# Performance work log

Measured on AMD Instinct MI355X. Metric: run time of the kernel, lower is better.

Reference implementation:

```python
import jax, jax.numpy as jnp
import numpy as np

B, T = 32, 64
DETER, HID, STOCH, CLASSES = 2048, 1024, 32, 32
ACT, EMB, BLOCKS = 16, 1024, 8
FLAT = STOCH * CLASSES
DPB = DETER // BLOCKS
DYN_IN_PB = DPB + 3 * HID
EPS = 1e-6
UNIMIX = 0.01


def _rms(x, g):
    return x * jax.lax.rsqrt(jnp.mean(x * x, axis=-1, keepdims=True) + EPS) * g


def _block_linear(x, W, b):
    # x: [N, BLOCKS*in_pb], W: [BLOCKS, in_pb, out_pb] -> [N, BLOCKS*out_pb]
    xg = x.reshape(x.shape[0], BLOCKS, -1)
    y = jnp.einsum('nbi,bio->nbo', xg, W)
    return y.reshape(x.shape[0], -1) + b


def setup_inputs() -> dict:
    key = jax.random.key(0)
    ks = iter(jax.random.split(key, 64))
    def lin(i, o):
        return jax.random.normal(next(ks), (i, o), jnp.float32) / np.float32(np.sqrt(i))
    inp = {}
    inp['embed'] = jax.random.normal(next(ks), (B, T, EMB), jnp.float32)
    inp['action'] = jax.random.normal(next(ks), (B, T, ACT), jnp.float32)
    inp['is_first'] = jax.random.randint(next(ks), (B, T), 0, 2).astype(jnp.int32)
    inp['W_in_deter'] = lin(DETER, HID); inp['b_in_deter'] = jnp.zeros((HID,), jnp.float32); inp['g_in_deter'] = jnp.ones((HID,), jnp.float32)
    inp['W_in_stoch'] = lin(FLAT, HID); inp['b_in_stoch'] = jnp.zeros((HID,), jnp.float32); inp['g_in_stoch'] = jnp.ones((HID,), jnp.float32)
    inp['W_in_act'] = lin(ACT, HID); inp['b_in_act'] = jnp.zeros((HID,), jnp.float32); inp['g_in_act'] = jnp.ones((HID,), jnp.float32)
    inp['W_dyn'] = jax.random.normal(next(ks), (BLOCKS, DYN_IN_PB, DPB), jnp.float32) / np.float32(np.sqrt(DYN_IN_PB))
    inp['b_dyn'] = jnp.zeros((DETER,), jnp.float32); inp['g_dyn'] = jnp.ones((DETER,), jnp.float32)
    inp['W_gru'] = jax.random.normal(next(ks), (BLOCKS, DPB, 3 * DPB), jnp.float32) / np.float32(np.sqrt(DPB))
    inp['b_gru'] = jnp.zeros((3 * DETER,), jnp.float32)
    inp['W_p0'] = lin(DETER, HID); inp['b_p0'] = jnp.zeros((HID,), jnp.float32); inp['g_p0'] = jnp.ones((HID,), jnp.float32)
    inp['W_p1'] = lin(HID, HID); inp['b_p1'] = jnp.zeros((HID,), jnp.float32); inp['g_p1'] = jnp.ones((HID,), jnp.float32)
    inp['W_po'] = jax.random.uniform(next(ks), (HID, FLAT), jnp.float32, -1.0, 1.0) / np.float32(np.sqrt(HID))
    inp['b_po'] = jnp.zeros((FLAT,), jnp.float32)
    inp['W_q0'] = lin(DETER + EMB, HID); inp['b_q0'] = jnp.zeros((HID,), jnp.float32); inp['g_q0'] = jnp.ones((HID,), jnp.float32)
    inp['W_qo'] = jax.random.uniform(next(ks), (HID, FLAT), jnp.float32, -1.0, 1.0) / np.float32(np.sqrt(HID))
    inp['b_qo'] = jnp.zeros((FLAT,), jnp.float32)
    return inp


def reference(embed, action, is_first,
              W_in_deter, b_in_deter, g_in_deter,
              W_in_stoch, b_in_stoch, g_in_stoch,
              W_in_act, b_in_act, g_in_act,
              W_dyn, b_dyn, g_dyn, W_gru, b_gru,
              W_p0, b_p0, g_p0, W_p1, b_p1, g_p1, W_po, b_po,
              W_q0, b_q0, g_q0, W_qo, b_qo):

    def core(deter, stoch_flat, act):
        denom = jax.lax.stop_gradient(jnp.maximum(jnp.abs(act), 1.0))
        a = act / denom
        x0 = jax.nn.silu(_rms(deter @ W_in_deter + b_in_deter, g_in_deter))
        x1 = jax.nn.silu(_rms(stoch_flat @ W_in_stoch + b_in_stoch, g_in_stoch))
        x2 = jax.nn.silu(_rms(a @ W_in_act + b_in_act, g_in_act))
        x = jnp.concatenate([x0, x1, x2], axis=-1)  # [B, 3H]
        xb = jnp.broadcast_to(x[:, None, :], (x.shape[0], BLOCKS, 3 * HID))
        dg = deter.reshape(-1, BLOCKS, DPB)
        h = jnp.concatenate([dg, xb], axis=-1).reshape(x.shape[0], -1)
        h = jax.nn.silu(_rms(_block_linear(h, W_dyn, b_dyn), g_dyn))
        gates = _block_linear(h, W_gru, b_gru).reshape(-1, BLOCKS, 3 * DPB)
        r = jax.nn.sigmoid(gates[..., :DPB])
        c = jnp.tanh(r * gates[..., DPB:2 * DPB])
        u = jax.nn.sigmoid(gates[..., 2 * DPB:] - 1.0)
        return (u * c + (1.0 - u) * dg).reshape(-1, DETER)

    def prior(deter):
        x = jax.nn.silu(_rms(deter @ W_p0 + b_p0, g_p0))
        x = jax.nn.silu(_rms(x @ W_p1 + b_p1, g_p1))
        return (x @ W_po + b_po).reshape(-1, STOCH, CLASSES)

    def post(deter, emb):
        x = jnp.concatenate([deter, emb], axis=-1)
        x = jax.nn.silu(_rms(x @ W_q0 + b_q0, g_q0))
        return (x @ W_qo + b_qo).reshape(-1, STOCH, CLASSES)

    def mode_st(logits):
        # unimix categorical, deterministic mode with straight-through gradients
        probs = (1.0 - UNIMIX) * jax.nn.softmax(logits, axis=-1) + UNIMIX / CLASSES
        onehot = jax.nn.one_hot(jnp.argmax(probs, axis=-1), CLASSES, dtype=probs.dtype)
        return onehot + probs - jax.lax.stop_gradient(probs)

    def step(carry, xs):
        deter, stoch = carry
        emb_t, act_t, first_t = xs
        m = (1.0 - first_t.astype(jnp.float32))[:, None]
        deter = deter * m
        stoch = stoch * m
        act_t = act_t * m
        deter = core(deter, stoch, act_t)
        prior_logits = prior(deter)
        post_logits = post(deter, emb_t)
        stoch = mode_st(post_logits).reshape(-1, FLAT)
        return (deter, stoch), (post_logits, prior_logits, deter)

    carry0 = (jnp.zeros((B, DETER), embed.dtype), jnp.zeros((B, FLAT), embed.dtype))
    xs = (embed.transpose(1, 0, 2), action.transpose(1, 0, 2), is_first.T)
    _, (post_l, prior_l, deters) = jax.lax.scan(step, carry0, xs)
    return (post_l.transpose(1, 0, 2, 3), prior_l.transpose(1, 0, 2, 3), deters.transpose(1, 0, 2))
```

## Files before the change

kernel.cpp:

```cpp
#include <hip/hip_runtime.h>
#include <math.h>

#define DEVINL __device__ __forceinline__
typedef float f32x4 __attribute__((ext_vector_type(4)));


struct RPtrs {
  const float *embed, *action; const int *is_first;
  const float *W_in_deter, *b_in_deter, *g_in_deter;
  const float *W_in_stoch, *b_in_stoch, *g_in_stoch;
  const float *W_in_act,   *b_in_act,   *g_in_act;
  const float *W_dyn, *b_dyn, *g_dyn;
  const float *W_gru, *b_gru;
  const float *W_p0, *b_p0, *g_p0;
  const float *W_p1, *b_p1, *g_p1;
  const float *W_po, *b_po;
  const float *W_q0, *b_q0, *g_q0;
  const float *W_qo, *b_qo;
  float *out_post, *out_prior, *out_deters;
  float *deter, *determ, *xact, *hact, *q0act;
  float *SDyn, *SQ0, *SX0, *SQO, *Abuf0, *Abuf1;
};

struct LdPlain {
  const float* A; int lda;
  DEVINL const float* addr(int r, int k) const { return A + (size_t)r * lda + k; }
};
struct LdDyn {
  const float* dm; const float* x; int blk;
  DEVINL const float* addr(int r, int k) const {
    return (k < 256) ? dm + (size_t)r * 2048 + blk * 256 + k
                     : x + (size_t)r * 3072 + (k - 256);
  }
};
struct LdQ0 {
  const float* det; const float* emb; int t;
  DEVINL const float* addr(int r, int k) const {
    return (k < 2048) ? det + (size_t)r * 2048 + k
                      : emb + ((size_t)r * 64 + t) * 1024 + (k - 2048);
  }
};

#define FMA4(A, S, W) { (A)[0]=fmaf((S),(W)[0],(A)[0]); (A)[1]=fmaf((S),(W)[1],(A)[1]); \
                        (A)[2]=fmaf((S),(W)[2],(A)[2]); (A)[3]=fmaf((S),(W)[3],(A)[3]); }

template <int NBLK, typename LA>
DEVINL void gemm_tile(LA la, const float* __restrict__ W, int ldw, int wcb,
                      int k0, float* __restrict__ slab, int sst, int scb,
                      const float* __restrict__ bias, float* As) {
  const int tid = threadIdx.x;
  const int c4 = (tid & 63) * 4;
  const int rg = (tid >> 6) * 8;
  const int srr = tid & 31;
  const int skk = (tid >> 5) * 8;
  f32x4 acc[8];
#pragma unroll
  for (int i = 0; i < 8; ++i) acc[i] = (f32x4){0.f, 0.f, 0.f, 0.f};
  const float* ap = la.addr(srr, k0 + skk);
  f32x4 cur0 = *(const f32x4*)ap;
  f32x4 cur1 = *(const f32x4*)(ap + 4);
#pragma unroll
  for (int b = 0; b < NBLK; ++b) {
    __syncthreads();
#pragma unroll
    for (int e = 0; e < 4; ++e) {
      As[(skk + e) * 36 + srr]     = cur0[e];
      As[(skk + 4 + e) * 36 + srr] = cur1[e];
    }
    f32x4 nxt0, nxt1;
    if (b + 1 < NBLK) {
      const float* np = la.addr(srr, k0 + (b + 1) * 64 + skk);
      nxt0 = *(const f32x4*)np;
      nxt1 = *(const f32x4*)(np + 4);
    }
    __syncthreads();
    const float* Wp = W + (size_t)(k0 + b * 64) * ldw + wcb + c4;
#pragma unroll 8
    for (int kk = 0; kk < 64; ++kk) {
      f32x4 w = *(const f32x4*)(Wp + (size_t)kk * ldw);
      const float* Ab = As + kk * 36 + rg;
      f32x4 alo = *(const f32x4*)(Ab);
      f32x4 ahi = *(const f32x4*)(Ab + 4);
      FMA4(acc[0], alo[0], w); FMA4(acc[1], alo[1], w);
      FMA4(acc[2], alo[2], w); FMA4(acc[3], alo[3], w);
      FMA4(acc[4], ahi[0], w); FMA4(acc[5], ahi[1], w);
      FMA4(acc[6], ahi[2], w); FMA4(acc[7], ahi[3], w);
    }
    if (b + 1 < NBLK) { cur0 = nxt0; cur1 = nxt1; }
  }
  f32x4 bv = (f32x4){0.f, 0.f, 0.f, 0.f};
  if (bias) bv = *(const f32x4*)(bias + wcb + c4);
#pragma unroll
  for (int i = 0; i < 8; ++i) {
    f32x4 o = acc[i] + bv;
    *(f32x4*)(slab + (size_t)(rg + i) * sst + scb + c4) = o;
  }
}

template <typename LA>
DEVINL void gemm_big(LA la, const float* __restrict__ W, int ldw, int wcb,
                     int nblk, float* __restrict__ outp, int ost,
                     const float* __restrict__ bias, float* As) {
  const int tid = threadIdx.x;
  const int c4 = (tid & 63) * 4;
  const int rg = (tid >> 6) * 8;
  const int srr = tid & 31;
  const int skk = (tid >> 5) * 8;
  f32x4 acc[8];
#pragma unroll
  for (int i = 0; i < 8; ++i) acc[i] = (f32x4){0.f, 0.f, 0.f, 0.f};
  const float* ap = la.addr(srr, skk);
  f32x4 cur0 = *(const f32x4*)ap;
  f32x4 cur1 = *(const f32x4*)(ap + 4);
  f32x4 nxt0, nxt1;
  for (int b = 0; b < nblk; ++b) {
    __syncthreads();
#pragma unroll
    for (int e = 0; e < 4; ++e) {
      As[(skk + e) * 36 + srr]     = cur0[e];
      As[(skk + 4 + e) * 36 + srr] = cur1[e];
    }
    if (b + 1 < nblk) {
      const float* np = la.addr(srr, (b + 1) * 64 + skk);
      nxt0 = *(const f32x4*)np;
      nxt1 = *(const f32x4*)(np + 4);
    }
    __syncthreads();
    const float* Wp = W + (size_t)(b * 64) * ldw + wcb + c4;
#pragma unroll 8
    for (int kk = 0; kk < 64; ++kk) {
      f32x4 w = *(const f32x4*)(Wp + (size_t)kk * ldw);
      const float* Ab = As + kk * 36 + rg;
      f32x4 alo = *(const f32x4*)(Ab);
      f32x4 ahi = *(const f32x4*)(Ab + 4);
      FMA4(acc[0], alo[0], w); FMA4(acc[1], alo[1], w);
      FMA4(acc[2], alo[2], w); FMA4(acc[3], alo[3], w);
      FMA4(acc[4], ahi[0], w); FMA4(acc[5], ahi[1], w);
      FMA4(acc[6], ahi[2], w); FMA4(acc[7], ahi[3], w);
    }
    if (b + 1 < nblk) { cur0 = nxt0; cur1 = nxt1; }
  }
  f32x4 bv = *(const f32x4*)(bias + wcb + c4);
#pragma unroll
  for (int i = 0; i < 8; ++i) {
    f32x4 o = acc[i] + bv;
    *(f32x4*)(outp + (size_t)(rg + i) * ost + wcb + c4) = o;
  }
}

DEVINL void act_fin(const float* __restrict__ slab, int N, int nch, int r,
                    const float* __restrict__ g, float* __restrict__ out,
                    float invN, float* red) {
  const int tid = threadIdx.x;
  const size_t cstr = (size_t)32 * N;
  const float* base = slab + (size_t)r * N + tid * 4;
  f32x4 y0 = (f32x4){0.f, 0.f, 0.f, 0.f}, y1 = y0;
  for (int ch = 0; ch < nch; ++ch)
    y0 += *(const f32x4*)(base + (size_t)ch * cstr);
  float ss = y0[0]*y0[0] + y0[1]*y0[1] + y0[2]*y0[2] + y0[3]*y0[3];
  if (N == 2048) {
    for (int ch = 0; ch < nch; ++ch)
      y1 += *(const f32x4*)(base + 1024 + (size_t)ch * cstr);
    ss += y1[0]*y1[0] + y1[1]*y1[1] + y1[2]*y1[2] + y1[3]*y1[3];
  }
#pragma unroll
  for (int o = 32; o > 0; o >>= 1) ss += __shfl_down(ss, o, 64);
  if ((tid & 63) == 0) red[tid >> 6] = ss;
  __syncthreads();
  if (tid == 0)
    red[4] = 1.f / sqrtf((red[0] + red[1] + red[2] + red[3]) * invN + 1e-6f);
  __syncthreads();
  const float sc = red[4];
  {
    f32x4 gg = *(const f32x4*)(g + tid * 4);
    f32x4 v = y0 * sc * gg;
#pragma unroll
    for (int k = 0; k < 4; ++k) v[k] = v[k] / (1.f + expf(-v[k]));
    *(f32x4*)(out + tid * 4) = v;
  }
  if (N == 2048) {
    f32x4 gg = *(const f32x4*)(g + 1024 + tid * 4);
    f32x4 v = y1 * sc * gg;
#pragma unroll
    for (int k = 0; k < 4; ++k) v[k] = v[k] / (1.f + expf(-v[k]));
    *(f32x4*)(out + 1024 + tid * 4) = v;
  }
}

DEVINL float sigm(float x) { return 1.f / (1.f + expf(-x)); }

DEVINL void x2_row(const RPtrs& p, int tt, int r, float m, float* red) {
  const int tid = threadIdx.x;
  const int c0 = tid * 4;
  const float* arow = p.action + ((size_t)r * 64 + tt) * 16;
  f32x4 s2 = *(const f32x4*)(p.b_in_act + c0);
#pragma unroll
  for (int ii = 0; ii < 16; ++ii) {
    float av = arow[ii] * m;
    av = av / fmaxf(fabsf(av), 1.f);
    f32x4 wv = *(const f32x4*)(p.W_in_act + ii * 1024 + c0);
    FMA4(s2, av, wv);
  }
  float ss = s2[0]*s2[0] + s2[1]*s2[1] + s2[2]*s2[2] + s2[3]*s2[3];
#pragma unroll
  for (int o = 32; o > 0; o >>= 1) ss += __shfl_down(ss, o, 64);
  if ((tid & 63) == 0) red[tid >> 6] = ss;
  __syncthreads();
  if (tid == 0)
    red[4] = 1.f / sqrtf((red[0] + red[1] + red[2] + red[3]) * (1.f / 1024.f) + 1e-6f);
  __syncthreads();
  float sc = red[4];
  f32x4 gg = *(const f32x4*)(p.g_in_act + c0);
  f32x4 v = s2 * sc * gg;
#pragma unroll
  for (int k = 0; k < 4; ++k) v[k] = v[k] / (1.f + expf(-v[k]));
  *(f32x4*)(p.xact + (size_t)r * 3072 + 2048 + c0) = v;
}

__global__ __launch_bounds__(256) void k_init(RPtrs p) {
  size_t i = (size_t)blockIdx.x * 256 + threadIdx.x;
  if (i < 65536) { p.deter[i] = 0.f; p.determ[i] = 0.f; }
}

__global__ __launch_bounds__(256, 2) void k_x0p(RPtrs p) {
  __shared__ __align__(16) float As[2304];
  int ct = blockIdx.x & 3, kc = blockIdx.x >> 2;
  LdPlain la{p.determ, 2048};
  gemm_tile<2>(la, p.W_in_deter, 1024, ct * 256, kc * 128,
               p.SX0 + (size_t)kc * 32768, 1024, ct * 256,
               kc == 0 ? p.b_in_deter : nullptr, As);
}

__global__ __launch_bounds__(256, 2) void k_profin(RPtrs p) {
  __shared__ float red[8];
  const int wg = blockIdx.x;
  const int tid = threadIdx.x;
  if (wg < 32) {
    act_fin(p.SX0, 1024, 16, wg, p.g_in_deter, p.xact + (size_t)wg * 3072,
            1.f / 1024.f, red);
  } else {
    const int r = wg - 32;
    const int c0 = tid * 4;
    f32x4 pre = *(const f32x4*)(p.b_in_stoch + c0);
    float ss = pre[0]*pre[0] + pre[1]*pre[1] + pre[2]*pre[2] + pre[3]*pre[3];
#pragma unroll
    for (int o = 32; o > 0; o >>= 1) ss += __shfl_down(ss, o, 64);
    if ((tid & 63) == 0) red[tid >> 6] = ss;
    __syncthreads();
    if (tid == 0)
      red[4] = 1.f / sqrtf((red[0] + red[1] + red[2] + red[3]) * (1.f / 1024.f) + 1e-6f);
    __syncthreads();
    float sc = red[4];
    f32x4 gg = *(const f32x4*)(p.g_in_stoch + c0);
    f32x4 v = pre * sc * gg;
#pragma unroll
    for (int k = 0; k < 4; ++k) v[k] = v[k] / (1.f + expf(-v[k]));
    *(f32x4*)(p.xact + (size_t)r * 3072 + 1024 + c0) = v;
    __syncthreads();
    float m = p.is_first[r * 64] ? 0.f : 1.f;
    x2_row(p, 0, r, m, red);
  }
}

__global__ __launch_bounds__(256, 2) void k_dyn(RPtrs p, int t) {
  __shared__ __align__(16) float As[2304];
  const int wg = blockIdx.x;
  int blk = wg / 26, kc = wg % 26;
  LdDyn la{p.determ, p.xact, blk};
  gemm_tile<2>(la, p.W_dyn + (size_t)blk * 851968, 256, 0, kc * 128,
               p.SDyn + (size_t)kc * 65536, 2048, blk * 256,
               kc == 0 ? p.b_dyn + blk * 256 : nullptr, As);
}

__global__ __launch_bounds__(256, 2) void k_dynfin(RPtrs p) {
  __shared__ float red[8];
  act_fin(p.SDyn, 2048, 26, blockIdx.x, p.g_dyn,
          p.hact + (size_t)blockIdx.x * 2048, 1.f / 2048.f, red);
}

__global__ __launch_bounds__(256, 2) void k_gru(RPtrs p, int t) {
  __shared__ float Al[8704];
  const int wg = blockIdx.x;
  const int blk = wg >> 4, jch = wg & 15;
  const int tid = threadIdx.x;
  {
    const float* hp = p.hact + blk * 256 + tid;
#pragma unroll
    for (int jb = 0; jb < 32; ++jb)
      Al[tid * 34 + jb] = hp[(size_t)jb * 2048];
  }
  __syncthreads();
  const int j = tid & 15, rg = tid >> 4;
  const int r0 = rg * 2;
  const int jcol = jch * 16 + j;
  const float* Wg = p.W_gru + (size_t)blk * 196608 + jcol;
  float r0a = 0, r1a = 0, c0a = 0, c1a = 0, u0a = 0, u1a = 0;
#pragma unroll 4
  for (int kk = 0; kk < 256; ++kk) {
    float wr = Wg[(size_t)kk * 768];
    float wc = Wg[(size_t)kk * 768 + 256];
    float wu = Wg[(size_t)kk * 768 + 512];
    float ax = Al[kk * 34 + r0], ay = Al[kk * 34 + r0 + 1];
    r0a = fmaf(ax, wr, r0a); r1a = fmaf(ay, wr, r1a);
    c0a = fmaf(ax, wc, c0a); c1a = fmaf(ay, wc, c1a);
    u0a = fmaf(ax, wu, u0a); u1a = fmaf(ay, wu, u1a);
  }
  const int col = blk * 256 + jcol;
  const float br = p.b_gru[blk * 768 + jcol];
  const float bc = p.b_gru[blk * 768 + 256 + jcol];
  const float bu = p.b_gru[blk * 768 + 512 + jcol];
#pragma unroll
  for (int rr = 0; rr < 2; ++rr) {
    int r = r0 + rr;
    float gr = (rr ? r1a : r0a) + br;
    float gc = (rr ? c1a : c0a) + bc;
    float gu = (rr ? u1a : u0a) + bu;
    float rs = sigm(gr);
    float cc = tanhf(rs * gc);
    float uu = sigm(gu - 1.f);
    float dg = p.determ[(size_t)r * 2048 + col];
    float nd = uu * cc + (1.f - uu) * dg;
    p.deter[(size_t)r * 2048 + col] = nd;
    p.out_deters[((size_t)r * 64 + t) * 2048 + col] = nd;
    float mn = 0.f;
    if (t + 1 < 64) mn = p.is_first[r * 64 + (t + 1)] ? 0.f : 1.f;
    p.determ[(size_t)r * 2048 + col] = nd * mn;
  }
}

__global__ __launch_bounds__(256, 2) void k_q0x0(RPtrs p, int t) {
  __shared__ __align__(16) float As[2304];
  const int wg = blockIdx.x;
  if (wg < 96) {
    int ct = wg & 3, kc = wg >> 2;
    LdQ0 la{p.deter, p.embed, t};
    gemm_tile<2>(la, p.W_q0, 1024, ct * 256, kc * 128,
                 p.SQ0 + (size_t)kc * 32768, 1024, ct * 256,
                 kc == 0 ? p.b_q0 : nullptr, As);
  } else {
    if (t >= 63) return;
    int i = wg - 96, ct = i & 3, kc = i >> 2;
    LdPlain la{p.determ, 2048};
    gemm_tile<2>(la, p.W_in_deter, 1024, ct * 256, kc * 128,
                 p.SX0 + (size_t)kc * 32768, 1024, ct * 256,
                 kc == 0 ? p.b_in_deter : nullptr, As);
  }
}

__global__ __launch_bounds__(256, 2) void k_qfin(RPtrs p, int t) {
  __shared__ float red[8];
  const int wg = blockIdx.x;
  if (wg < 32)
    act_fin(p.SQ0, 1024, 24, wg, p.g_q0, p.q0act + (size_t)wg * 1024,
            1.f / 1024.f, red);
  else {
    if (t >= 63) return;
    act_fin(p.SX0, 1024, 16, wg - 32, p.g_in_deter,
            p.xact + (size_t)(wg - 32) * 3072, 1.f / 1024.f, red);
  }
}

__global__ __launch_bounds__(256, 2) void k_qo(RPtrs p, int t) {
  __shared__ __align__(16) float As[2304];
  int ct = blockIdx.x & 3, kc = blockIdx.x >> 2;
  LdPlain la{p.q0act, 1024};
  gemm_tile<1>(la, p.W_qo, 1024, ct * 256, kc * 64,
               p.SQO + (size_t)kc * 32768, 1024, ct * 256,
               kc == 0 ? p.b_qo : nullptr, As);
}

__global__ __launch_bounds__(256, 2) void k_finx12(RPtrs p, int t) {
  __shared__ __align__(16) float ybuf[1024];
  __shared__ float red[8];
  __shared__ int sidx[32];
  const int r = blockIdx.x;
  const int tid = threadIdx.x;
  const float* b0 = p.SQO + (size_t)r * 1024 + tid * 4;
  f32x4 y = (f32x4){0.f, 0.f, 0.f, 0.f};
#pragma unroll
  for (int ch = 0; ch < 16; ++ch) y += *(const f32x4*)(b0 + (size_t)ch * 32768);
  *(f32x4*)(p.out_post + ((size_t)r * 64 + t) * 1024 + tid * 4) = y;
  *(f32x4*)(ybuf + tid * 4) = y;
  __syncthreads();
  if (tid < 32) {
    const float* rb = ybuf + tid * 32;
    float best = rb[0]; int bi = 0;
#pragma unroll
    for (int c = 1; c < 32; ++c) {
      float v = rb[c];
      if (v > best) { best = v; bi = c; }
    }
    sidx[tid] = bi;
  }
  __syncthreads();
  if (t >= 63) return;
  const float m = p.is_first[r * 64 + t + 1] ? 0.f : 1.f;
  const int c0 = tid * 4;
  f32x4 s1 = (f32x4){0.f, 0.f, 0.f, 0.f};
  if (m != 0.f) {
    for (int g = 0; g < 32; ++g)
      s1 += *(const f32x4*)(p.W_in_stoch + (size_t)(g * 32 + sidx[g]) * 1024 + c0);
  }
  f32x4 pre = *(const f32x4*)(p.b_in_stoch + c0) + s1 * m;
  float ss = pre[0]*pre[0] + pre[1]*pre[1] + pre[2]*pre[2] + pre[3]*pre[3];
#pragma unroll
  for (int o = 32; o > 0; o >>= 1) ss += __shfl_down(ss, o, 64);
  if ((tid & 63) == 0) red[tid >> 6] = ss;
  __syncthreads();
  if (tid == 0)
    red[4] = 1.f / sqrtf((red[0] + red[1] + red[2] + red[3]) * (1.f / 1024.f) + 1e-6f);
  __syncthreads();
  {
    float sc = red[4];
    f32x4 gg = *(const f32x4*)(p.g_in_stoch + c0);
    f32x4 v = pre * sc * gg;
#pragma unroll
    for (int k = 0; k < 4; ++k) v[k] = v[k] / (1.f + expf(-v[k]));
    *(f32x4*)(p.xact + (size_t)r * 3072 + 1024 + c0) = v;
  }
  __syncthreads();
  x2_row(p, t + 1, r, m, red);
}

__global__ __launch_bounds__(256, 2) void kb_p0(RPtrs p) {
  __shared__ __align__(16) float As[2304];
  int rb = blockIdx.x >> 2, ct = blockIdx.x & 3;
  LdPlain la{p.out_deters + (size_t)rb * 32 * 2048, 2048};
  gemm_big(la, p.W_p0, 1024, ct * 256, 32,
           p.Abuf0 + (size_t)rb * 32 * 1024, 1024, p.b_p0, As);
}
__global__ __launch_bounds__(256, 2) void kb_fin0(RPtrs p) {
  __shared__ float red[8];
  int r = blockIdx.x;
  act_fin(p.Abuf0, 1024, 1, r, p.g_p0, p.Abuf1 + (size_t)r * 1024,
          1.f / 1024.f, red);
}
__global__ __launch_bounds__(256, 2) void kb_p1(RPtrs p) {
  __shared__ __align__(16) float As[2304];
  int rb = blockIdx.x >> 2, ct = blockIdx.x & 3;
  LdPlain la{p.Abuf1 + (size_t)rb * 32 * 1024, 1024};
  gemm_big(la, p.W_p1, 1024, ct * 256, 16,
           p.Abuf0 + (size_t)rb * 32 * 1024, 1024, p.b_p1, As);
}
__global__ __launch_bounds__(256, 2) void kb_fin1(RPtrs p) {
  __shared__ float red[8];
  int r = blockIdx.x;
  act_fin(p.Abuf0, 1024, 1, r, p.g_p1, p.Abuf1 + (size_t)r * 1024,
          1.f / 1024.f, red);
}
__global__ __launch_bounds__(256, 2) void kb_po(RPtrs p) {
  __shared__ __align__(16) float As[2304];
  int rb = blockIdx.x >> 2, ct = blockIdx.x & 3;
  LdPlain la{p.Abuf1 + (size_t)rb * 32 * 1024, 1024};
  gemm_big(la, p.W_po, 1024, ct * 256, 16,
           p.out_prior + (size_t)rb * 32 * 1024, 1024, p.b_po, As);
}

extern "C" void kernel_launch(void* const* d_in, const int* in_sizes, int n_in,
                              void* d_out, int out_size, void* d_ws,
                              size_t ws_size, hipStream_t stream) {
  RPtrs p;
  p.embed      = (const float*)d_in[0];
  p.action     = (const float*)d_in[1];
  p.is_first   = (const int*)d_in[2];
  p.W_in_deter = (const float*)d_in[3];  p.b_in_deter = (const float*)d_in[4];  p.g_in_deter = (const float*)d_in[5];
  p.W_in_stoch = (const float*)d_in[6];  p.b_in_stoch = (const float*)d_in[7];  p.g_in_stoch = (const float*)d_in[8];
  p.W_in_act   = (const float*)d_in[9];  p.b_in_act   = (const float*)d_in[10]; p.g_in_act   = (const float*)d_in[11];
  p.W_dyn      = (const float*)d_in[12]; p.b_dyn      = (const float*)d_in[13]; p.g_dyn      = (const float*)d_in[14];
  p.W_gru      = (const float*)d_in[15]; p.b_gru      = (const float*)d_in[16];
  p.W_p0       = (const float*)d_in[17]; p.b_p0       = (const float*)d_in[18]; p.g_p0       = (const float*)d_in[19];
  p.W_p1       = (const float*)d_in[20]; p.b_p1       = (const float*)d_in[21]; p.g_p1       = (const float*)d_in[22];
  p.W_po       = (const float*)d_in[23]; p.b_po       = (const float*)d_in[24];
  p.W_q0       = (const float*)d_in[25]; p.b_q0       = (const float*)d_in[26]; p.g_q0       = (const float*)d_in[27];
  p.W_qo       = (const float*)d_in[28]; p.b_qo       = (const float*)d_in[29];

  float* o = (float*)d_out;
  p.out_post   = o;
  p.out_prior  = o + 2097152;
  p.out_deters = o + 4194304;

  float* w = (float*)d_ws;
  p.deter  = w;
  p.determ = w + 65536;
  p.xact   = w + 131072;
  p.hact   = w + 229376;
  p.q0act  = w + 294912;
  p.SDyn   = w + 393216;
  p.SQ0    = w + 2097152;
  p.SX0    = w + 2883584;
  p.SQO    = w + 3407872;
  p.Abuf0  = w;
  p.Abuf1  = w + 2097152;

  k_init<<<512, 256, 0, stream>>>(p);
  k_x0p<<<64, 256, 0, stream>>>(p);
  k_profin<<<64, 256, 0, stream>>>(p);
  for (int t = 0; t < 64; ++t) {
    k_dyn<<<208, 256, 0, stream>>>(p, t);
    k_dynfin<<<32, 256, 0, stream>>>(p);
    k_gru<<<128, 256, 0, stream>>>(p, t);
    k_q0x0<<<160, 256, 0, stream>>>(p, t);
    k_qfin<<<64, 256, 0, stream>>>(p, t);
    k_qo<<<64, 256, 0, stream>>>(p, t);
    k_finx12<<<32, 256, 0, stream>>>(p, t);
  }
  kb_p0<<<256, 256, 0, stream>>>(p);
  kb_fin0<<<2048, 256, 0, stream>>>(p);
  kb_p1<<<256, 256, 0, stream>>>(p);
  kb_fin1<<<2048, 256, 0, stream>>>(p);
  kb_po<<<256, 256, 0, stream>>>(p);
}
```

Baseline: 7.257 ms.

## Fuse q-finalize, qo projection and stoch update into one per-row kernel

Merges the q0 RMS-norm finalize, the W_qo projection and the argmax/stoch embedding step into a single kernel per batch row. The qo projection becomes a per-row matrix-vector loop instead of a split-K GEMM with a partial-sum buffer. The initial x0 GEMM on zero state is replaced by computing the activation straight from the bias inside the init kernel. This cuts launches and intermediate buffers per timestep, but each of only 32 blocks now streams all of W_qo serially, which may lengthen the critical path.

```diff
diff --git a/kernel.cpp b/kernel.cpp
--- a/kernel.cpp
+++ b/kernel.cpp
@@ -18,8 +18,8 @@
   const float *W_q0, *b_q0, *g_q0;
   const float *W_qo, *b_qo;
   float *out_post, *out_prior, *out_deters;
-  float *deter, *determ, *xact, *hact, *q0act;
-  float *SDyn, *SQ0, *SX0, *SQO, *Abuf0, *Abuf1;
+  float *deter, *determ, *xact, *hact;
+  float *SDyn, *SQ0, *SX0, *Abuf0, *Abuf1;
 };
 
 struct LdPlain {
@@ -217,45 +217,37 @@
   *(f32x4*)(p.xact + (size_t)r * 3072 + 2048 + c0) = v;
 }
 
+DEVINL void bias_row(const float* __restrict__ b, const float* __restrict__ g,
+                     float* __restrict__ out, float* red) {
+  const int tid = threadIdx.x;
+  const int c0 = tid * 4;
+  f32x4 pre = *(const f32x4*)(b + c0);
+  float ss = pre[0]*pre[0] + pre[1]*pre[1] + pre[2]*pre[2] + pre[3]*pre[3];
+#pragma unroll
+  for (int o = 32; o > 0; o >>= 1) ss += __shfl_down(ss, o, 64);
+  if ((tid & 63) == 0) red[tid >> 6] = ss;
+  __syncthreads();
+  if (tid == 0)
+    red[4] = 1.f / sqrtf((red[0] + red[1] + red[2] + red[3]) * (1.f / 1024.f) + 1e-6f);
+  __syncthreads();
+  float sc = red[4];
+  f32x4 gg = *(const f32x4*)(g + c0);
+  f32x4 v = pre * sc * gg;
+#pragma unroll
+  for (int k = 0; k < 4; ++k) v[k] = v[k] / (1.f + expf(-v[k]));
+  *(f32x4*)(out + c0) = v;
+}
+
 __global__ __launch_bounds__(256) void k_init(RPtrs p) {
-  size_t i = (size_t)blockIdx.x * 256 + threadIdx.x;
-  if (i < 65536) { p.deter[i] = 0.f; p.determ[i] = 0.f; }
-}
-
-__global__ __launch_bounds__(256, 2) void k_x0p(RPtrs p) {
-  __shared__ __align__(16) float As[2304];
-  int ct = blockIdx.x & 3, kc = blockIdx.x >> 2;
-  LdPlain la{p.determ, 2048};
-  gemm_tile<2>(la, p.W_in_deter, 1024, ct * 256, kc * 128,
-               p.SX0 + (size_t)kc * 32768, 1024, ct * 256,
-               kc == 0 ? p.b_in_deter : nullptr, As);
-}
-
-__global__ __launch_bounds__(256, 2) void k_profin(RPtrs p) {
   __shared__ float red[8];
   const int wg = blockIdx.x;
-  const int tid = threadIdx.x;
-  if (wg < 32) {
-    act_fin(p.SX0, 1024, 16, wg, p.g_in_deter, p.xact + (size_t)wg * 3072,
-            1.f / 1024.f, red);
-  } else {
-    const int r = wg - 32;
-    const int c0 = tid * 4;
-    f32x4 pre = *(const f32x4*)(p.b_in_stoch + c0);
-    float ss = pre[0]*pre[0] + pre[1]*pre[1] + pre[2]*pre[2] + pre[3]*pre[3];
-#pragma unroll
-    for (int o = 32; o > 0; o >>= 1) ss += __shfl_down(ss, o, 64);
-    if ((tid & 63) == 0) red[tid >> 6] = ss;
-    __syncthreads();
-    if (tid == 0)
-      red[4] = 1.f / sqrtf((red[0] + red[1] + red[2] + red[3]) * (1.f / 1024.f) + 1e-6f);
-    __syncthreads();
-    float sc = red[4];
-    f32x4 gg = *(const f32x4*)(p.g_in_stoch + c0);
-    f32x4 v = pre * sc * gg;
-#pragma unroll
-    for (int k = 0; k < 4; ++k) v[k] = v[k] / (1.f + expf(-v[k]));
-    *(f32x4*)(p.xact + (size_t)r * 3072 + 1024 + c0) = v;
+  size_t i = (size_t)wg * 256 + threadIdx.x;
+  if (i < 65536) { p.deter[i] = 0.f; p.determ[i] = 0.f; }
+  if (wg >= 480) {
+    const int r = wg - 480;
+    bias_row(p.b_in_deter, p.g_in_deter, p.xact + (size_t)r * 3072, red);
+    __syncthreads();
+    bias_row(p.b_in_stoch, p.g_in_stoch, p.xact + (size_t)r * 3072 + 1024, red);
     __syncthreads();
     float m = p.is_first[r * 64] ? 0.f : 1.f;
     x2_row(p, 0, r, m, red);
@@ -347,41 +339,55 @@
   }
 }
 
-__global__ __launch_bounds__(256, 2) void k_qfin(RPtrs p, int t) {
+__global__ __launch_bounds__(256, 2) void k_mega(RPtrs p, int t) {
+  __shared__ __align__(16) float qrow[1024];
+  __shared__ __align__(16) float ybuf[1024];
   __shared__ float red[8];
+  __shared__ int sidx[32];
   const int wg = blockIdx.x;
-  if (wg < 32)
-    act_fin(p.SQ0, 1024, 24, wg, p.g_q0, p.q0act + (size_t)wg * 1024,
-            1.f / 1024.f, red);
-  else {
+  const int tid = threadIdx.x;
+  if (wg >= 32) {
     if (t >= 63) return;
     act_fin(p.SX0, 1024, 16, wg - 32, p.g_in_deter,
             p.xact + (size_t)(wg - 32) * 3072, 1.f / 1024.f, red);
-  }
-}
-
-__global__ __launch_bounds__(256, 2) void k_qo(RPtrs p, int t) {
-  __shared__ __align__(16) float As[2304];
-  int ct = blockIdx.x & 3, kc = blockIdx.x >> 2;
-  LdPlain la{p.q0act, 1024};
-  gemm_tile<1>(la, p.W_qo, 1024, ct * 256, kc * 64,
-               p.SQO + (size_t)kc * 32768, 1024, ct * 256,
-               kc == 0 ? p.b_qo : nullptr, As);
-}
-
-__global__ __launch_bounds__(256, 2) void k_finx12(RPtrs p, int t) {
-  __shared__ __align__(16) float ybuf[1024];
-  __shared__ float red[8];
-  __shared__ int sidx[32];
-  const int r = blockIdx.x;
-  const int tid = threadIdx.x;
-  const float* b0 = p.SQO + (size_t)r * 1024 + tid * 4;
-  f32x4 y = (f32x4){0.f, 0.f, 0.f, 0.f};
-#pragma unroll
-  for (int ch = 0; ch < 16; ++ch) y += *(const f32x4*)(b0 + (size_t)ch * 32768);
-  *(f32x4*)(p.out_post + ((size_t)r * 64 + t) * 1024 + tid * 4) = y;
-  *(f32x4*)(ybuf + tid * 4) = y;
-  __syncthreads();
+    return;
+  }
+  const int r = wg;
+  const int c0 = tid * 4;
+  {
+    const float* base = p.SQ0 + (size_t)r * 1024 + c0;
+    f32x4 y = (f32x4){0.f, 0.f, 0.f, 0.f};
+#pragma unroll
+    for (int ch = 0; ch < 24; ++ch) y += *(const f32x4*)(base + (size_t)ch * 32768);
+    float ss = y[0]*y[0] + y[1]*y[1] + y[2]*y[2] + y[3]*y[3];
+#pragma unroll
+    for (int o = 32; o > 0; o >>= 1) ss += __shfl_down(ss, o, 64);
+    if ((tid & 63) == 0) red[tid >> 6] = ss;
+    __syncthreads();
+    if (tid == 0)
+      red[4] = 1.f / sqrtf((red[0] + red[1] + red[2] + red[3]) * (1.f / 1024.f) + 1e-6f);
+    __syncthreads();
+    float sc = red[4];
+    f32x4 gg = *(const f32x4*)(p.g_q0 + c0);
+    f32x4 v = y * sc * gg;
+#pragma unroll
+    for (int k = 0; k < 4; ++k) v[k] = v[k] / (1.f + expf(-v[k]));
+    *(f32x4*)(qrow + c0) = v;
+  }
+  __syncthreads();
+  {
+    f32x4 acc = *(const f32x4*)(p.b_qo + c0);
+    const float* Wq = p.W_qo + c0;
+#pragma unroll 8
+    for (int k = 0; k < 1024; ++k) {
+      f32x4 wv = *(const f32x4*)(Wq + (size_t)k * 1024);
+      FMA4(acc, qrow[k], wv);
+    }
+    *(f32x4*)(p.out_post + ((size_t)r * 64 + t) * 1024 + c0) = acc;
+    *(f32x4*)(ybuf + c0) = acc;
+  }
+  __syncthreads();
+  if (t >= 63) return;
   if (tid < 32) {
     const float* rb = ybuf + tid * 32;
     float best = rb[0]; int bi = 0;
@@ -393,24 +399,22 @@
     sidx[tid] = bi;
   }
   __syncthreads();
-  if (t >= 63) return;
   const float m = p.is_first[r * 64 + t + 1] ? 0.f : 1.f;
-  const int c0 = tid * 4;
-  f32x4 s1 = (f32x4){0.f, 0.f, 0.f, 0.f};
-  if (m != 0.f) {
-    for (int g = 0; g < 32; ++g)
-      s1 += *(const f32x4*)(p.W_in_stoch + (size_t)(g * 32 + sidx[g]) * 1024 + c0);
-  }
-  f32x4 pre = *(const f32x4*)(p.b_in_stoch + c0) + s1 * m;
-  float ss = pre[0]*pre[0] + pre[1]*pre[1] + pre[2]*pre[2] + pre[3]*pre[3];
-#pragma unroll
-  for (int o = 32; o > 0; o >>= 1) ss += __shfl_down(ss, o, 64);
-  if ((tid & 63) == 0) red[tid >> 6] = ss;
-  __syncthreads();
-  if (tid == 0)
-    red[4] = 1.f / sqrtf((red[0] + red[1] + red[2] + red[3]) * (1.f / 1024.f) + 1e-6f);
-  __syncthreads();
   {
+    f32x4 s1 = (f32x4){0.f, 0.f, 0.f, 0.f};
+    if (m != 0.f) {
+      for (int g = 0; g < 32; ++g)
+        s1 += *(const f32x4*)(p.W_in_stoch + (size_t)(g * 32 + sidx[g]) * 1024 + c0);
+    }
+    f32x4 pre = *(const f32x4*)(p.b_in_stoch + c0) + s1 * m;
+    float ss = pre[0]*pre[0] + pre[1]*pre[1] + pre[2]*pre[2] + pre[3]*pre[3];
+#pragma unroll
+    for (int o = 32; o > 0; o >>= 1) ss += __shfl_down(ss, o, 64);
+    if ((tid & 63) == 0) red[tid >> 6] = ss;
+    __syncthreads();
+    if (tid == 0)
+      red[4] = 1.f / sqrtf((red[0] + red[1] + red[2] + red[3]) * (1.f / 1024.f) + 1e-6f);
+    __syncthreads();
     float sc = red[4];
     f32x4 gg = *(const f32x4*)(p.g_in_stoch + c0);
     f32x4 v = pre * sc * gg;
@@ -484,25 +488,19 @@
   p.determ = w + 65536;
   p.xact   = w + 131072;
   p.hact   = w + 229376;
-  p.q0act  = w + 294912;
   p.SDyn   = w + 393216;
   p.SQ0    = w + 2097152;
   p.SX0    = w + 2883584;
-  p.SQO    = w + 3407872;
   p.Abuf0  = w;
   p.Abuf1  = w + 2097152;
 
   k_init<<<512, 256, 0, stream>>>(p);
-  k_x0p<<<64, 256, 0, stream>>>(p);
-  k_profin<<<64, 256, 0, stream>>>(p);
   for (int t = 0; t < 64; ++t) {
     k_dyn<<<208, 256, 0, stream>>>(p, t);
     k_dynfin<<<32, 256, 0, stream>>>(p);
     k_gru<<<128, 256, 0, stream>>>(p, t);
     k_q0x0<<<160, 256, 0, stream>>>(p, t);
-    k_qfin<<<64, 256, 0, stream>>>(p, t);
-    k_qo<<<64, 256, 0, stream>>>(p, t);
-    k_finx12<<<32, 256, 0, stream>>>(p, t);
+    k_mega<<<64, 256, 0, stream>>>(p, t);
   }
   kb_p0<<<256, 256, 0, stream>>>(p);
   kb_fin0<<<2048, 256, 0, stream>>>(p);
```

After: 9.439 ms. 30.1% more time.
